# Optimization experiments

Measured on AMD Instinct MI355X. Metric: run time of the kernel, lower is better.

Reference implementation:

```python
import jax, jax.numpy as jnp
import numpy as np
from jax import lax

BN_EPS = 1e-5


def _gcn_layer(X, edge_index, W, sW, sb, gamma, beta):
    # X: (B, T, V, Fin). Self-loop linear + per-edge message + scatter-add.
    H = X @ sW + sb  # (B, T, V, Hd)
    src = edge_index[:, 0]
    dst = edge_index[:, 1]
    msgs = X[:, :, src, :] @ W  # (B, T, E, Hd) gather + GEMM
    H = H + jnp.zeros_like(H).at[:, :, dst, :].add(msgs)  # scatter-add over dst
    # BatchNorm1d applied per timestep in the torch loop -> stats over (B, V) per t
    mean = H.mean(axis=(0, 2), keepdims=True)
    var = H.var(axis=(0, 2), keepdims=True)  # biased var, as torch train-mode BN
    H = (H - mean) * lax.rsqrt(var + BN_EPS) * gamma + beta
    return jax.nn.relu(H)


def _conv_bn_relu(x, w, b, gamma, beta, dilation, padding):
    # x: (B, C, T), w: (O, I, K)
    y = lax.conv_general_dilated(x, w, window_strides=(1,),
                                 padding=[(padding, padding)],
                                 rhs_dilation=(dilation,),
                                 dimension_numbers=('NCH', 'OIH', 'NCH'))
    y = y + b[None, :, None]
    mean = y.mean(axis=(0, 2), keepdims=True)
    var = y.var(axis=(0, 2), keepdims=True)
    y = (y - mean) * lax.rsqrt(var + BN_EPS) * gamma[None, :, None] + beta[None, :, None]
    return jax.nn.relu(y)


def setup_inputs() -> dict:
    key = jax.random.key(0)
    ks = jax.random.split(key, 16)
    B, C, T, V, Hd, E, NC = 64, 3, 512, 25, 64, 48, 60
    s = 0.05
    inp = {
        'X': jax.random.normal(ks[0], (B, C, T, V), jnp.float32),
        'edge_index': jax.random.randint(ks[1], (E, 2), 0, V, jnp.int32),
        'W1': jax.random.normal(ks[2], (C, Hd), jnp.float32) * s,
        's1W': jax.random.normal(ks[3], (C, Hd), jnp.float32) * s,
        's1b': jax.random.normal(ks[4], (Hd,), jnp.float32) * s,
        'g1': jnp.ones((Hd,), jnp.float32),
        'b1': jnp.zeros((Hd,), jnp.float32),
        'W2': jax.random.normal(ks[5], (Hd, Hd), jnp.float32) * s,
        's2W': jax.random.normal(ks[6], (Hd, Hd), jnp.float32) * s,
        's2b': jax.random.normal(ks[7], (Hd,), jnp.float32) * s,
        'g2': jnp.ones((Hd,), jnp.float32),
        'b2': jnp.zeros((Hd,), jnp.float32),
        'c1W': jax.random.normal(ks[8], (64, V * Hd, 3), jnp.float32) * s,
        'c1b': jax.random.normal(ks[9], (64,), jnp.float32) * s,
        'tg1': jnp.ones((64,), jnp.float32),
        'tb1': jnp.zeros((64,), jnp.float32),
        'c2W': jax.random.normal(ks[10], (128, 64, 3), jnp.float32) * s,
        'c2b': jax.random.normal(ks[11], (128,), jnp.float32) * s,
        'tg2': jnp.ones((128,), jnp.float32),
        'tb2': jnp.zeros((128,), jnp.float32),
        'fcW': jax.random.normal(ks[12], (128, NC), jnp.float32) * s,
        'fcb': jax.random.normal(ks[13], (NC,), jnp.float32) * s,
    }
    return inp


def reference(X, edge_index, W1, s1W, s1b, g1, b1, W2, s2W, s2b, g2, b2,
              c1W, c1b, tg1, tb1, c2W, c2b, tg2, tb2, fcW, fcb):
    B, C, T, V = X.shape
    Xt = jnp.transpose(X, (0, 2, 3, 1))  # (B, T, V, C)
    H = _gcn_layer(Xt, edge_index, W1, s1W, s1b, g1, b1)  # (B, T, V, Hd)
    H = _gcn_layer(H, edge_index, W2, s2W, s2b, g2, b2)   # (B, T, V, Hd)
    Hd = H.shape[-1]
    # permute(0,2,3,1).reshape(B, V*Hd, T)
    z = jnp.transpose(H, (0, 2, 3, 1)).reshape(B, V * Hd, T)
    z = _conv_bn_relu(z, c1W, c1b, tg1, tb1, dilation=1, padding=1)
    z = _conv_bn_relu(z, c2W, c2b, tg2, tb2, dilation=2, padding=2)
    z = z.mean(axis=2)  # (B, 128)
    return z @ fcW + fcb
```

## Files before the change

### kernel.cpp

```cpp
#include <hip/hip_runtime.h>
#include <hip/hip_bf16.h>
#include <cstddef>

using bf16 = __hip_bfloat16;
typedef __attribute__((ext_vector_type(4)))  short bf16x4;
typedef __attribute__((ext_vector_type(8)))  short bf16x8;
typedef __attribute__((ext_vector_type(4)))  float f32x4;
typedef __attribute__((ext_vector_type(16))) float f32x16;
typedef __attribute__((ext_vector_type(2)))  unsigned int uint32x2;
typedef __attribute__((ext_vector_type(4)))  unsigned int uint32x4;

#define B_   64
#define T_   512
#define V_   25
#define HD_  64
#define E_   48
#define NC_  60

__device__ __forceinline__ bf16  f2b(float x){ return __float2bfloat16(x); }
__device__ __forceinline__ unsigned short f2bits(float x){ return __builtin_bit_cast(unsigned short, f2b(x)); }
__device__ __forceinline__ float bits2f(unsigned short s){ return __builtin_bit_cast(float, ((unsigned)s)<<16); }
__device__ __forceinline__ float rbf(float x){ return bits2f(f2bits(x)); }
__device__ __forceinline__ unsigned cvtpk(float lo, float hi){
  unsigned r;
  asm("v_cvt_pk_bf16_f32 %0, %1, %2" : "=v"(r) : "v"(lo), "v"(hi));
  return r;
}
__device__ __forceinline__ short cvt1(float x){ return (short)(unsigned short)cvtpk(x, x); }

__global__ void k_wt(const float* __restrict__ c1W, const float* __restrict__ c2W,
                     const float* __restrict__ s2W, const float* __restrict__ W2,
                     const float* __restrict__ s1W, const float* __restrict__ W1,
                     const int* __restrict__ ei,
                     bf16* __restrict__ Wb, bf16* __restrict__ Wb2,
                     bf16* __restrict__ WbB, bf16* __restrict__ W6f,
                     int* __restrict__ offs, int* __restrict__ lst)
{
  int i0 = blockIdx.x*blockDim.x + threadIdx.x, stride = gridDim.x*blockDim.x;
  if(blockIdx.x == 0 && threadIdx.x == 0){
    int cnt[V_], pos[V_];
    for(int v=0;v<V_;v++) cnt[v]=0;
    for(int e=0;e<E_;e++) cnt[ei[2*e+1]]++;
    int off = 0;
    for(int v=0;v<V_;v++){ offs[v]=off; pos[v]=off; off+=cnt[v]; }
    offs[V_] = off;
    for(int e=0;e<E_;e++){ int d = ei[2*e+1]; lst[pos[d]++] = ei[2*e+0]; }
  }
  for(int i = i0; i < 307200; i += stride){
    int hlo = i & 15, o = (i>>4)&63, kc = (i>>10)%12, v = i/12288;
    int ks = kc>>2, h = (kc&3)*16 + hlo;
    Wb[i] = f2b(c1W[(o*1600 + v*64 + h)*3 + ks]);
  }
  for(int i = i0; i < 24576; i += stride){
    int hlo = i & 15, o = (i>>4)&127, kc = i>>11;
    int ks = kc>>2, c = (kc&3)*16 + hlo;
    Wb2[i] = f2b(c2W[(o*64 + c)*3 + ks]);
  }
  for(int i = i0; i < 8192; i += stride){
    int j = i&7, l=(i>>3)&63, n=(i>>9)&3, kt=i>>11;
    int k = kt*32 + (l>>4)*8 + j;
    int h = n*16 + (l&15);
    float val = (k < 64) ? s2W[k*64 + h] : W2[(k-64)*64 + h];
    WbB[i] = f2b(val);
  }
  for(int i = i0; i < 2048; i += stride){
    int j = i&7, l=(i>>3)&63, n=(i>>9)&3;
    int k = (l>>4)*8 + j, h = n*16 + (l&15);
    float val = 0.f;
    if(k < 3) val = s1W[k*64 + h];
    else if(k < 6) val = W1[(k-3)*64 + h];
    W6f[i] = f2b(val);
  }
}

__global__ __launch_bounds__(512) void k_stats1(
    const float* __restrict__ X,
    const int* __restrict__ offs, const int* __restrict__ lst,
    float* __restrict__ gpart)
{
  int tid = threadIdx.x;
  int b = blockIdx.y, t0 = blockIdx.x*16;
  __shared__ short Xs[1248];
  __shared__ short Z6[3200];
  __shared__ unsigned char soc[32], slc[48];

  if(tid < V_+1) soc[tid] = (unsigned char)offs[tid];
  else if(tid >= 64 && tid < 64+E_) slc[tid-64] = (unsigned char)lst[tid-64];
  for(int i=tid; i<1248; i+=512){
    int c = i/416, r = i - c*416, tl = r/26, v = r - tl*26;
    short val = 0;
    if(v < 25) val = cvt1(X[((size_t)(b*3+c)*T_ + t0+tl)*V_ + v]);
    Xs[i] = val;
  }
  __syncthreads();
  if(tid < 400){
    int v = tid>>4, tl = tid&15, xb = tl*26;
    float a0=0.f, a1=0.f, a2=0.f;
    int e1 = soc[v+1];
    for(int e=soc[v]; e<e1; e++){
      int u = slc[e];
      a0 += bits2f((unsigned short)Xs[xb+u]);
      a1 += bits2f((unsigned short)Xs[416+xb+u]);
      a2 += bits2f((unsigned short)Xs[832+xb+u]);
    }
    unsigned p01 = cvtpk(a0, a1);
    bf16x8 z;
    z[0]=Xs[xb+v]; z[1]=Xs[416+xb+v]; z[2]=Xs[832+xb+v];
    z[3]=(short)p01; z[4]=(short)(p01>>16); z[5]=cvt1(a2);
    z[6]=0; z[7]=0;
    *(bf16x8*)&Z6[tid*8] = z;
  }
  __syncthreads();

  int t = tid>>5, item = tid&31;
  if(item < 27){
    int k = item, kk = -1;
    if(item >= 6){
      int r = item - 6; k = 0;
      while(r >= 6-k){ r -= 6-k; k++; }
      kk = k + r;
    }
    float acc = 0.f;
    for(int v=0;v<25;v++){
      const short* z = &Z6[(v*16 + t)*8];
      float a = bits2f((unsigned short)z[k]);
      if(kk < 0) acc += a;
      else acc += a * bits2f((unsigned short)z[kk]);
    }
    gpart[((size_t)blockIdx.x*64 + b)*432 + t*27 + item] = acc;
  }
}

__global__ __launch_bounds__(256) void k_bnfin1(
    const float* __restrict__ gpart,
    const float* __restrict__ s1W, const float* __restrict__ W1,
    const float* __restrict__ g, const float* __restrict__ bt,
    float* __restrict__ scale, float* __restrict__ shift)
{
  int tid = threadIdx.x;
  int t0 = blockIdx.x*4;
  int tx = t0 >> 4, tlb = t0 & 15;
  __shared__ float SM[4][27];
  __shared__ float Wsh[6][64];
  for(int i=tid; i<108; i+=256){
    int tl = i/27, item = i%27;
    float s = 0.f;
    for(int b=0;b<64;b++)
      s += gpart[((size_t)tx*64 + b)*432 + (tlb+tl)*27 + item];
    SM[tl][item] = s;
  }
  for(int i=tid; i<384; i+=256){
    int k = i>>6, h = i&63;
    float w = (k<3) ? s1W[k*64+h] : W1[(k-3)*64+h];
    Wsh[k][h] = rbf(w);
  }
  __syncthreads();
  int tl = tid>>6, h = tid&63;
  float w[6];
  #pragma unroll
  for(int k=0;k<6;k++) w[k] = Wsh[k][h];
  float lin = 0.f;
  #pragma unroll
  for(int k=0;k<6;k++) lin += w[k]*SM[tl][k];
  float qq = 0.f;
  int idx = 6;
  #pragma unroll
  for(int k=0;k<6;k++){
    #pragma unroll 6
    for(int kk=k;kk<6;kk++){
      float c = w[k]*w[kk];
      if(kk != k) c += c;
      qq += c*SM[tl][idx++];
    }
  }
  float m = lin * (1.0f/1600.0f);
  float v = qq * (1.0f/1600.0f) - m*m;
  float r = rsqrtf(fmaxf(v, 0.f) + 1e-5f);
  float sc = g[h]*r;
  scale[(t0+tl)*64 + h] = sc;
  shift[(t0+tl)*64 + h] = bt[h] - m*sc;
}

__global__ void k_bnfin_th(const float* __restrict__ part,
                           const float* __restrict__ g, const float* __restrict__ bt,
                           float* __restrict__ scale, float* __restrict__ shift)
{
  int i = blockIdx.x*blockDim.x + threadIdx.x;
  if(i < T_*HD_){
    int h = i & 63, t = i >> 6, bx = t >> 4, tl = t & 15;
    const float* p = part + ((size_t)bx*64)*2048 + tl*64 + h;
    float s = 0.f, q = 0.f;
    for(int b=0;b<64;b++){ s += p[(size_t)b*2048]; q += p[(size_t)b*2048 + 1024]; }
    float m = s * (1.0f/1600.0f);
    float v = q * (1.0f/1600.0f) - m*m;
    float r = rsqrtf(fmaxf(v, 0.f) + 1e-5f);
    float sc = g[h]*r;
    scale[i] = sc;
    shift[i] = bt[h] - m*sc;
  }
}

__global__ __launch_bounds__(512,4) void k_gcn2(
    const float* __restrict__ X,
    const float* __restrict__ scale1, const float* __restrict__ shift1,
    const bf16* __restrict__ W6f, const bf16* __restrict__ WbB,
    const int* __restrict__ offs, const int* __restrict__ lst,
    unsigned char* __restrict__ Hout, float* __restrict__ part)
{
  int tid = threadIdx.x, lane = tid & 63, wid = tid >> 6;
  int b = blockIdx.y, t0 = blockIdx.x*16;
  __shared__ short Zs[400*72];
  __shared__ short WbBs[8192];
  __shared__ unsigned int pss[1024];
  __shared__ unsigned char soc[32], slc[48];
  short* Z6 = Zs;
  short* Xs = Zs + 3200;

  bf16x8 w6[4];
  #pragma unroll
  for(int n=0;n<4;n++) w6[n] = *(const bf16x8*)&W6f[(n*64 + lane)*8];

  if(tid < V_+1) soc[tid] = (unsigned char)offs[tid];
  else if(tid >= 64 && tid < 64+E_) slc[tid-64] = (unsigned char)lst[tid-64];
  for(int i=tid; i<1024; i+=512){
    pss[i] = ((unsigned)f2bits(shift1[t0*64+i])<<16) | f2bits(scale1[t0*64+i]);
    *(bf16x8*)&WbBs[i*8] = *(const bf16x8*)&WbB[i*8];
  }
  for(int i=tid; i<1248; i+=512){
    int c = i/416, r = i - c*416, tl = r/26, v = r - tl*26;
    short val = 0;
    if(v < 25) val = cvt1(X[((size_t)(b*3+c)*T_ + t0+tl)*V_ + v]);
    Xs[i] = val;
  }
  __syncthreads();

  if(tid < 400){
    int v = tid>>4, tl = tid&15, xb = tl*26;
    float a0=0.f, a1=0.f, a2=0.f;
    int e1 = soc[v+1];
    for(int e=soc[v]; e<e1; e++){
      int u = slc[e];
      a0 += bits2f((unsigned short)Xs[xb+u]);
      a1 += bits2f((unsigned short)Xs[416+xb+u]);
      a2 += bits2f((unsigned short)Xs[832+xb+u]);
    }
    unsigned p01 = cvtpk(a0, a1);
    bf16x8 z;
    z[0]=Xs[xb+v]; z[1]=Xs[416+xb+v]; z[2]=Xs[832+xb+v];
    z[3]=(short)p01; z[4]=(short)(p01>>16); z[5]=cvt1(a2);
    z[6]=0; z[7]=0;
    *(bf16x8*)&Z6[tid*8] = z;
  }
  __syncthreads();

  f32x4 c1f[4][4] = {};
  #pragma unroll
  for(int vi=0; vi<4; vi++){
    int v = wid + vi*8;
    if(v < V_){
      bf16x8 af = {0,0,0,0,0,0,0,0};
      if(lane < 16) af = *(const bf16x8*)&Z6[(v*16 + lane)*8];
      #pragma unroll
      for(int n=0;n<4;n++)
        c1f[vi][n] = __builtin_amdgcn_mfma_f32_16x16x32_bf16(af, w6[n], c1f[vi][n], 0, 0, 0);
    }
  }
  __syncthreads();

  int l15 = lane & 15, tlb = (lane>>4)*4;
  #pragma unroll
  for(int vi=0; vi<4; vi++){
    int v = wid + vi*8;
    if(v < V_){
      #pragma unroll
      for(int n=0;n<4;n++){
        float y[4];
        #pragma unroll
        for(int j=0;j<4;j++){
          unsigned u = pss[(tlb+j)*64 + n*16 + l15];
          y[j] = fmaxf(c1f[vi][n][j]*bits2f((unsigned short)(u&0xffffu)) + bits2f((unsigned short)(u>>16)), 0.f);
        }
        unsigned p01 = cvtpk(y[0], y[1]), p23 = cvtpk(y[2], y[3]);
        short* base = &Zs[(v*16 + tlb)*72 + n*16 + l15];
        base[0]   = (short)p01;  base[72]  = (short)(p01>>16);
        base[144] = (short)p23;  base[216] = (short)(p23>>16);
      }
    }
  }
  __syncthreads();

  int cg = (lane>>4)*8;
  f32x4 accs[4][4] = {};
  #pragma unroll
  for(int vi=0; vi<4; vi++){
    int v = wid + vi*8;
    if(v < V_){
      const short* rowp = &Zs[(v*16 + l15)*72 + cg];
      bf16x8 a0 = *(const bf16x8*)rowp;
      bf16x8 a1 = *(const bf16x8*)(rowp + 32);
      float s0[8]={0,0,0,0,0,0,0,0}, s1[8]={0,0,0,0,0,0,0,0};
      int e1 = soc[v+1];
      for(int e=soc[v]; e<e1; e++){
        int u = slc[e];
        const short* np = &Zs[(u*16 + l15)*72 + cg];
        bf16x8 n0 = *(const bf16x8*)np;
        bf16x8 n1 = *(const bf16x8*)(np + 32);
        #pragma unroll
        for(int j=0;j<8;j++){ s0[j] += bits2f((unsigned short)n0[j]); s1[j] += bits2f((unsigned short)n1[j]); }
      }
      uint32x4 ua2, ua3;
      #pragma unroll
      for(int j=0;j<4;j++){ ua2[j] = cvtpk(s0[2*j], s0[2*j+1]); ua3[j] = cvtpk(s1[2*j], s1[2*j+1]); }
      bf16x8 a2 = __builtin_bit_cast(bf16x8, ua2);
      bf16x8 a3 = __builtin_bit_cast(bf16x8, ua3);
      #pragma unroll
      for(int n=0;n<4;n++){
        bf16x8 b0 = *(const bf16x8*)&WbBs[(( 0+n)*64 + lane)*8];
        accs[vi][n] = __builtin_amdgcn_mfma_f32_16x16x32_bf16(a0, b0, accs[vi][n], 0, 0, 0);
        bf16x8 b1 = *(const bf16x8*)&WbBs[(( 4+n)*64 + lane)*8];
        accs[vi][n] = __builtin_amdgcn_mfma_f32_16x16x32_bf16(a1, b1, accs[vi][n], 0, 0, 0);
        bf16x8 b2 = *(const bf16x8*)&WbBs[(( 8+n)*64 + lane)*8];
        accs[vi][n] = __builtin_amdgcn_mfma_f32_16x16x32_bf16(a2, b2, accs[vi][n], 0, 0, 0);
        bf16x8 b3 = *(const bf16x8*)&WbBs[((12+n)*64 + lane)*8];
        accs[vi][n] = __builtin_amdgcn_mfma_f32_16x16x32_bf16(a3, b3, accs[vi][n], 0, 0, 0);
      }
    }
  }
  __syncthreads();

  f32x4 ssum[4] = {}, ssq[4] = {};
  #pragma unroll
  for(int vi=0; vi<4; vi++){
    int v = wid + vi*8;
    if(v < V_){
      #pragma unroll
      for(int n=0;n<4;n++){
        float val[4];
        #pragma unroll
        for(int j=0;j<4;j++){
          val[j] = accs[vi][n][j];
          ssum[n][j] += val[j]; ssq[n][j] += val[j]*val[j];
        }
        unsigned p01 = cvtpk(val[0], val[1]), p23 = cvtpk(val[2], val[3]);
        short* base = &Zs[(tlb*25 + v)*72 + n*16 + l15];
        base[0]    = (short)p01;  base[1800] = (short)(p01>>16);
        base[3600] = (short)p23;  base[5400] = (short)(p23>>16);
      }
    }
  }
  __syncthreads();

  unsigned char* hbout = Hout + ((size_t)b*T_ + t0)*V_*64;
  for(int c=tid; c<3200; c+=512){
    bf16x8 o = *(const bf16x8*)&Zs[(c>>3)*72 + (c&7)*8];
    float f[8];
    #pragma unroll
    for(int j=0;j<8;j++) f[j] = bits2f((unsigned short)o[j]);
    int w0 = 0, w1 = 0;
    w0 = __builtin_amdgcn_cvt_pk_fp8_f32(f[0], f[1], w0, false);
    w0 = __builtin_amdgcn_cvt_pk_fp8_f32(f[2], f[3], w0, true);
    w1 = __builtin_amdgcn_cvt_pk_fp8_f32(f[4], f[5], w1, false);
    w1 = __builtin_amdgcn_cvt_pk_fp8_f32(f[6], f[7], w1, true);
    uint32x2 st; st.x = (unsigned)w0; st.y = (unsigned)w1;
    __builtin_nontemporal_store(st, (uint32x2*)&hbout[(size_t)c*8]);
  }
  __syncthreads();

  float* red = (float*)Zs;
  size_t pb = ((size_t)blockIdx.x*64 + blockIdx.y)*2048;
  #pragma unroll
  for(int n=0;n<4;n++)
    #pragma unroll
    for(int j=0;j<4;j++)
      red[wid*1024 + (tlb+j)*64 + n*16 + l15] = ssum[n][j];
  __syncthreads();
  for(int i=tid; i<1024; i+=512){
    float s = 0.f;
    #pragma unroll
    for(int w=0;w<8;w++) s += red[w*1024 + i];
    __builtin_nontemporal_store(s, &part[pb + i]);
  }
  __syncthreads();
  #pragma unroll
  for(int n=0;n<4;n++)
    #pragma unroll
    for(int j=0;j<4;j++)
      red[wid*1024 + (tlb+j)*64 + n*16 + l15] = ssq[n][j];
  __syncthreads();
  for(int i=tid; i<1024; i+=512){
    float q = 0.f;
    #pragma unroll
    for(int w=0;w<8;w++) q += red[w*1024 + i];
    __builtin_nontemporal_store(q, &part[pb + 1024 + i]);
  }
}

__device__ __forceinline__ uint32x2 loadH8(const unsigned char* H, int b, int v, int t0, int s){
  int ti = s>>3, h0 = (s&7)*8, t = t0-1+ti;
  uint32x2 r; r.x = 0u; r.y = 0u;
  if(t >= 0 && t < T_) r = *(const uint32x2*)&H[(((size_t)b*T_+t)*V_ + v)*HD_ + h0];
  return r;
}

__device__ __forceinline__ void xform_store(short* zbuf, const unsigned int* sshf, int s, uint32x2 raw){
  int ti = s>>3, h0 = (s&7)*8;
  uint4 u0 = *(const uint4*)&sshf[ti*64 + h0];
  uint4 u1 = *(const uint4*)&sshf[ti*64 + h0 + 4];
  unsigned int uu[8] = {u0.x,u0.y,u0.z,u0.w,u1.x,u1.y,u1.z,u1.w};
  float x[8];
  x[0] = __builtin_amdgcn_cvt_f32_fp8((int)raw.x, 0);
  x[1] = __builtin_amdgcn_cvt_f32_fp8((int)raw.x, 1);
  x[2] = __builtin_amdgcn_cvt_f32_fp8((int)raw.x, 2);
  x[3] = __builtin_amdgcn_cvt_f32_fp8((int)raw.x, 3);
  x[4] = __builtin_amdgcn_cvt_f32_fp8((int)raw.y, 0);
  x[5] = __builtin_amdgcn_cvt_f32_fp8((int)raw.y, 1);
  x[6] = __builtin_amdgcn_cvt_f32_fp8((int)raw.y, 2);
  x[7] = __builtin_amdgcn_cvt_f32_fp8((int)raw.y, 3);
  float r[8];
  #pragma unroll
  for(int j=0;j<8;j++){
    float scl = bits2f((unsigned short)(uu[j] & 0xffffu));
    float shf = bits2f((unsigned short)(uu[j] >> 16));
    r[j] = fmaxf(x[j]*scl + shf, 0.f);
  }
  uint32x4 u;
  #pragma unroll
  for(int j=0;j<4;j++) u[j] = cvtpk(r[2*j], r[2*j+1]);
  *(uint32x4*)&zbuf[ti*72 + h0] = u;
}

__global__ __launch_bounds__(256) void k_conv1(
    const unsigned char* __restrict__ H, const float* __restrict__ scale2, const float* __restrict__ shift2,
    const bf16* __restrict__ Wb, bf16* __restrict__ C1b, float* __restrict__ cpart1)
{
  int b = blockIdx.y, t0 = blockIdx.x*32, tid = threadIdx.x;
  int lane = tid & 63, w = tid >> 6;
  __shared__ unsigned int sshf[34*64];
  __shared__ short zs[2][2][34*72];

  for(int i = tid; i < 34*64; i += 256){
    int ti = i>>6, h = i&63, t = t0-1+ti;
    unsigned int u = 0;
    if(t >= 0 && t < T_){
      u = ((unsigned)f2bits(shift2[t*64+h])<<16) | f2bits(scale2[t*64+h]);
    }
    sshf[i] = u;
  }
  __syncthreads();

  {
    uint32x2 a0 = loadH8(H,b,0,t0,tid);
    uint32x2 b0 = loadH8(H,b,13,t0,tid);
    uint32x2 a1, b1; a1.x=a1.y=b1.x=b1.y=0u;
    if(tid<16){ a1 = loadH8(H,b,0,t0,tid+256); b1 = loadH8(H,b,13,t0,tid+256); }
    xform_store(&zs[0][0][0], sshf, tid, a0);
    xform_store(&zs[1][0][0], sshf, tid, b0);
    if(tid<16){ xform_store(&zs[0][0][0], sshf, tid+256, a1); xform_store(&zs[1][0][0], sshf, tid+256, b1); }
  }
  uint32x2 rA0 = loadH8(H,b,1,t0,tid), rB0 = loadH8(H,b,14,t0,tid);
  uint32x2 rA1, rB1; rA1.x=rA1.y=rB1.x=rB1.y=0u;
  if(tid<16){ rA1 = loadH8(H,b,1,t0,tid+256); rB1 = loadH8(H,b,14,t0,tid+256); }
  __syncthreads();

  int g = w >> 1;
  int o0 = (w & 1)*32;
  int vbase = g ? 13 : 0, nv = g ? 12 : 13;
  f32x16 acc = {};
  for(int i=0; i<13; i++){
    uint32x2 nA0, nA1, nB0, nB1;
    nA0.x=nA0.y=nA1.x=nA1.y=nB0.x=nB0.y=nB1.x=nB1.y=0u;
    if(i+2 < 13){
      nA0 = loadH8(H,b,i+2,t0,tid);
      if(tid<16) nA1 = loadH8(H,b,i+2,t0,tid+256);
    }
    if(i+2 < 12){
      nB0 = loadH8(H,b,13+i+2,t0,tid);
      if(tid<16) nB1 = loadH8(H,b,13+i+2,t0,tid+256);
    }
    if(i < nv){
      int v = vbase + i;
      const short* zbuf = &zs[g][i&1][0];
      #pragma unroll
      for(int kc=0; kc<12; kc++){
        int ks = kc>>2;
        bf16x8 af = *(const bf16x8*)&Wb[((v*12+kc)*64 + o0 + (lane&31))*16 + (lane>>5)*8];
        int row = (lane&31) + ks;
        int col = (kc&3)*16 + (lane>>5)*8;
        bf16x8 bfr = *(const bf16x8*)&zbuf[row*72 + col];
        acc = __builtin_amdgcn_mfma_f32_32x32x16_bf16(af, bfr, acc, 0, 0, 0);
      }
    }
    if(i+1 < 13){
      xform_store(&zs[0][(i+1)&1][0], sshf, tid, rA0);
      if(tid<16) xform_store(&zs[0][(i+1)&1][0], sshf, tid+256, rA1);
    }
    if(i+1 < 12){
      xform_store(&zs[1][(i+1)&1][0], sshf, tid, rB0);
      if(tid<16) xform_store(&zs[1][(i+1)&1][0], sshf, tid+256, rB1);
    }
    rA0=nA0; rA1=nA1; rB0=nB0; rB1=nB1;
    __syncthreads();
  }

  float* redB = (float*)&zs[0][0][0];
  short* Cs   = &zs[0][0][0] + 4224;
  if(g == 1){
    #pragma unroll
    for(int r=0;r<16;r++){
      int ol = (r&3) + 8*(r>>2) + 4*(lane>>5);
      redB[(w&1)*1056 + ol*33 + (lane&31)] = acc[r];
    }
  }
  __syncthreads();
  if(g == 0){
    #pragma unroll
    for(int r=0;r<16;r++){
      int ol = (r&3) + 8*(r>>2) + 4*(lane>>5);
      float val = acc[r] + redB[(w&1)*1056 + ol*33 + (lane&31)];
      Cs[((w&1)*32 + ol)*32 + (lane&31)] = cvt1(val);
    }
  }
  __syncthreads();

  {
    int o = tid>>2, tseg = (tid&3)*8;
    bf16x8 row = *(const bf16x8*)&Cs[o*32 + tseg];
    *(bf16x8*)&C1b[((size_t)b*64 + o)*T_ + t0 + tseg] = row;
  }
  if(tid < 64){
    float s = 0.f, q = 0.f;
    for(int t=0;t<32;t++){
      float v = bits2f((unsigned short)Cs[tid*32 + t]);
      s += v; q += v*v;
    }
    size_t pb = ((size_t)blockIdx.y*16 + blockIdx.x)*128;
    cpart1[pb + tid] = s;
    cpart1[pb + 64 + tid] = q;
  }
}

__global__ __launch_bounds__(256) void k_redch(const float* __restrict__ cpart,
    const float* __restrict__ g, const float* __restrict__ bt,
    float* __restrict__ scale, float* __restrict__ shift, int nch, int nblk, float inv_count)
{
  int o = blockIdx.x, tid = threadIdx.x;
  float s = 0.f, q = 0.f;
  for(int blk=tid; blk<nblk; blk+=256){
    s += cpart[(size_t)blk*2*nch + o];
    q += cpart[(size_t)blk*2*nch + nch + o];
  }
  for(int off=32; off; off>>=1){ s += __shfl_down(s, off); q += __shfl_down(q, off); }
  __shared__ float rs[4], rq[4];
  if((tid&63)==0){ rs[tid>>6]=s; rq[tid>>6]=q; }
  __syncthreads();
  if(tid==0){
    s = rs[0]+rs[1]+rs[2]+rs[3]; q = rq[0]+rq[1]+rq[2]+rq[3];
    float m = s*inv_count;
    float v = q*inv_count - m*m;
    float r = rsqrtf(fmaxf(v, 0.f) + 1e-5f);
    float sc = g[o]*r;
    scale[o] = sc; shift[o] = bt[o] - m*sc;
  }
}

__global__ __launch_bounds__(256) void k_conv2(
    const bf16* __restrict__ C1b, const float* __restrict__ scale3, const float* __restrict__ shift3,
    const bf16* __restrict__ Wb2, short* __restrict__ C2b, float* __restrict__ cpart)
{
  int b = blockIdx.y, t0 = blockIdx.x*64, tid = threadIdx.x;
  int lane = tid & 63, w = tid >> 6;
  __shared__ short zT[68*72];
  __shared__ float scl[64], shf[64];
  __shared__ float rpart[4][16][2][2];
  if(tid < 64){ scl[tid]=scale3[tid]; shf[tid]=shift3[tid]; }
  __syncthreads();
  for(int i=tid; i<4352; i+=256){
    int c = i/68, r = i%68, t = t0 - 2 + r;
    float val = 0.f;
    if(t >= 0 && t < T_) val = fmaxf(bits2f((unsigned short)__builtin_bit_cast(short, C1b[((size_t)b*64+c)*T_ + t]))*scl[c] + shf[c], 0.f);
    zT[r*72 + c] = cvt1(val);
  }
  __syncthreads();
  int o0 = w*32;
  float sr[16], qr[16];
  #pragma unroll
  for(int r=0;r<16;r++){ sr[r]=0.f; qr[r]=0.f; }
  #pragma unroll
  for(int tt=0; tt<2; tt++){
    int twv = tt*32;
    f32x16 acc = {};
    #pragma unroll
    for(int kc=0; kc<12; kc++){
      bf16x8 af = *(const bf16x8*)&Wb2[((kc*128) + o0 + (lane&31))*16 + (lane>>5)*8];
      bf16x8 bfr = *(const bf16x8*)&zT[(twv + (lane&31) + 2*(kc>>2))*72 + (kc&3)*16 + (lane>>5)*8];
      acc = __builtin_amdgcn_mfma_f32_32x32x16_bf16(af, bfr, acc, 0, 0, 0);
    }
    int t = t0 + twv + (lane&31);
    #pragma unroll
    for(int r=0;r<16;r++){
      int o = o0 + (r&3) + 8*(r>>2) + 4*(lane>>5);
      float y = acc[r];
      C2b[((size_t)b*128 + o)*T_ + t] = cvt1(y);
      sr[r] += y; qr[r] += y*y;
    }
  }
  #pragma unroll
  for(int r=0;r<16;r++){
    float s = sr[r], q = qr[r];
    #pragma unroll
    for(int m=1;m<=16;m<<=1){ s += __shfl_xor(s, m); q += __shfl_xor(q, m); }
    if((lane&31)==0){ rpart[w][r][lane>>5][0]=s; rpart[w][r][lane>>5][1]=q; }
  }
  __syncthreads();
  if(tid < 128){
    int wv = tid>>5, r = (tid>>1)&15, hf = tid&1;
    int o = wv*32 + (r&3) + 8*(r>>2) + 4*hf;
    size_t pb = ((size_t)(blockIdx.y*8 + blockIdx.x))*256;
    cpart[pb + o]       = rpart[wv][r][hf][0];
    cpart[pb + 128 + o] = rpart[wv][r][hf][1];
  }
}

__global__ __launch_bounds__(256) void k_head(
    const short* __restrict__ C2b, const float* __restrict__ scale4, const float* __restrict__ shift4,
    const float* __restrict__ fcW, const float* __restrict__ fcb, float* __restrict__ out)
{
  int b = blockIdx.x, tid = threadIdx.x;
  __shared__ float mean[128];
  __shared__ float ms[256];
  int ch = tid >> 1, p = tid & 1;
  float scl = scale4[ch], shf = shift4[ch];
  const short* src = C2b + ((size_t)b*128 + ch)*T_ + p*256;
  float s = 0.f;
  for(int i=0;i<32;i++){
    bf16x8 v8 = *(const bf16x8*)&src[i*8];
    #pragma unroll
    for(int j=0;j<8;j++) s += fmaxf(bits2f((unsigned short)v8[j])*scl + shf, 0.f);
  }
  ms[tid] = s;
  __syncthreads();
  if(tid < 128) mean[tid] = (ms[2*tid] + ms[2*tid+1]) * (1.0f/512.0f);
  __syncthreads();
  if(tid < NC_){
    float acc = fcb[tid];
    for(int c=0;c<128;c++) acc += mean[c]*fcW[c*NC_ + tid];
    out[b*NC_ + tid] = acc;
  }
}

extern "C" void kernel_launch(void* const* d_in, const int* in_sizes, int n_in,
                              void* d_out, int out_size, void* d_ws, size_t ws_size,
                              hipStream_t stream)
{
  const float* X   = (const float*)d_in[0];
  const int*   ei  = (const int*)  d_in[1];
  const float* W1  = (const float*)d_in[2];
  const float* s1W = (const float*)d_in[3];
  const float* g1  = (const float*)d_in[5];
  const float* b1  = (const float*)d_in[6];
  const float* W2  = (const float*)d_in[7];
  const float* s2W = (const float*)d_in[8];
  const float* g2  = (const float*)d_in[10];
  const float* b2  = (const float*)d_in[11];
  const float* c1W = (const float*)d_in[12];
  const float* tg1 = (const float*)d_in[14];
  const float* tb1 = (const float*)d_in[15];
  const float* c2W = (const float*)d_in[16];
  const float* tg2 = (const float*)d_in[18];
  const float* tb2 = (const float*)d_in[19];
  const float* fcW = (const float*)d_in[20];
  const float* fcb = (const float*)d_in[21];

  char* ws = (char*)d_ws;
  unsigned char* H = (unsigned char*)(ws);
  bf16*  C1b    = (bf16*) (ws + 104857600);
  float* cpart1 = (float*)(ws + 109051904);
  float* cpart2 = (float*)(ws + 109576192);
  float* part   = (float*)(ws + 113246208);
  float* gpart  = part;
  short* C2b    = (short*)part;
  bf16*  Wb     = (bf16*) (ws + 130023424);
  bf16*  Wb2    = (bf16*) (ws + 131252224);
  bf16*  WbB    = (bf16*) (ws + 131350528);
  float* stats  = (float*)(ws + 131366912);
  bf16*  W6f    = (bf16*) (stats);
  float* scale1 = stats + 131456; float* shift1 = scale1 + 32768;
  float* scale2 = shift1 + 32768; float* shift2 = scale2 + 32768;
  float* scale3 = shift2 + 32768; float* shift3 = scale3 + 64;
  float* scale4 = shift3 + 64;    float* shift4 = scale4 + 128;
  int* csr_off = (int*)(shift4 + 128);
  int* csr_lst = csr_off + 32;

  k_wt<<<256, 256, 0, stream>>>(c1W, c2W, s2W, W2, s1W, W1, ei, Wb, Wb2, WbB, W6f, csr_off, csr_lst);

  k_stats1<<<dim3(T_/16, B_), 512, 0, stream>>>(X, csr_off, csr_lst, gpart);
  k_bnfin1<<<128, 256, 0, stream>>>(gpart, s1W, W1, g1, b1, scale1, shift1);
  k_gcn2<<<dim3(T_/16, B_), 512, 0, stream>>>(X, scale1, shift1, W6f, WbB, csr_off, csr_lst, H, part);
  k_bnfin_th<<<128, 256, 0, stream>>>(part, g2, b2, scale2, shift2);
  k_conv1<<<dim3(16, B_), 256, 0, stream>>>(H, scale2, shift2, Wb, C1b, cpart1);
  k_redch<<<64, 256, 0, stream>>>(cpart1, tg1, tb1, scale3, shift3, 64, 1024, 1.0f/32768.0f);
  k_conv2<<<dim3(8, B_), 256, 0, stream>>>(C1b, scale3, shift3, Wb2, C2b, cpart2);
  k_redch<<<128, 256, 0, stream>>>(cpart2, tg2, tb2, scale4, shift4, 128, 512, 1.0f/32768.0f);
  k_head<<<B_, 256, 0, stream>>>(C2b, scale4, shift4, fcW, fcb, (float*)d_out);
}
```

Before: 201.9 us.

## Use LDS atomics for GCN stat reduction and split head kernel over time

Result: slower. 361.6 us (+79.1%).

```diff
diff --git a/kernel.cpp b/kernel.cpp
--- a/kernel.cpp
+++ b/kernel.cpp
@@ -367,32 +367,19 @@
   __syncthreads();
 
   float* red = (float*)Zs;
-  size_t pb = ((size_t)blockIdx.x*64 + blockIdx.y)*2048;
+  for(int i=tid; i<2048; i+=512) red[i] = 0.f;
+  __syncthreads();
   #pragma unroll
   for(int n=0;n<4;n++)
     #pragma unroll
-    for(int j=0;j<4;j++)
-      red[wid*1024 + (tlb+j)*64 + n*16 + l15] = ssum[n][j];
-  __syncthreads();
-  for(int i=tid; i<1024; i+=512){
-    float s = 0.f;
-    #pragma unroll
-    for(int w=0;w<8;w++) s += red[w*1024 + i];
-    __builtin_nontemporal_store(s, &part[pb + i]);
-  }
-  __syncthreads();
-  #pragma unroll
-  for(int n=0;n<4;n++)
-    #pragma unroll
-    for(int j=0;j<4;j++)
-      red[wid*1024 + (tlb+j)*64 + n*16 + l15] = ssq[n][j];
-  __syncthreads();
-  for(int i=tid; i<1024; i+=512){
-    float q = 0.f;
-    #pragma unroll
-    for(int w=0;w<8;w++) q += red[w*1024 + i];
-    __builtin_nontemporal_store(q, &part[pb + 1024 + i]);
-  }
+    for(int j=0;j<4;j++){
+      atomicAdd(&red[(tlb+j)*64 + n*16 + l15], ssum[n][j]);
+      atomicAdd(&red[1024 + (tlb+j)*64 + n*16 + l15], ssq[n][j]);
+    }
+  __syncthreads();
+  size_t pb = ((size_t)blockIdx.x*64 + blockIdx.y)*2048;
+  for(int i=tid; i<2048; i+=512)
+    __builtin_nontemporal_store(red[i], &part[pb + i]);
 }
 
 __device__ __forceinline__ uint32x2 loadH8(const unsigned char* H, int b, int v, int t0, int s){
@@ -621,25 +608,34 @@
   }
 }
 
-__global__ __launch_bounds__(256) void k_head(
+__global__ __launch_bounds__(256) void k_head1(
     const short* __restrict__ C2b, const float* __restrict__ scale4, const float* __restrict__ shift4,
-    const float* __restrict__ fcW, const float* __restrict__ fcb, float* __restrict__ out)
-{
-  int b = blockIdx.x, tid = threadIdx.x;
-  __shared__ float mean[128];
+    float* __restrict__ hpart)
+{
+  int b = blockIdx.y, q = blockIdx.x, tid = threadIdx.x;
   __shared__ float ms[256];
   int ch = tid >> 1, p = tid & 1;
   float scl = scale4[ch], shf = shift4[ch];
-  const short* src = C2b + ((size_t)b*128 + ch)*T_ + p*256;
+  const short* src = C2b + ((size_t)b*128 + ch)*T_ + q*128 + p*64;
   float s = 0.f;
-  for(int i=0;i<32;i++){
+  for(int i=0;i<8;i++){
     bf16x8 v8 = *(const bf16x8*)&src[i*8];
     #pragma unroll
     for(int j=0;j<8;j++) s += fmaxf(bits2f((unsigned short)v8[j])*scl + shf, 0.f);
   }
   ms[tid] = s;
   __syncthreads();
-  if(tid < 128) mean[tid] = (ms[2*tid] + ms[2*tid+1]) * (1.0f/512.0f);
+  if(tid < 128) hpart[((size_t)b*4 + q)*128 + tid] = ms[2*tid] + ms[2*tid+1];
+}
+
+__global__ __launch_bounds__(128) void k_head2(
+    const float* __restrict__ hpart, const float* __restrict__ fcW, const float* __restrict__ fcb,
+    float* __restrict__ out)
+{
+  int b = blockIdx.x, tid = threadIdx.x;
+  __shared__ float mean[128];
+  const float* hp = hpart + (size_t)b*512;
+  mean[tid] = (hp[tid] + hp[128+tid] + hp[256+tid] + hp[384+tid]) * (1.0f/512.0f);
   __syncthreads();
   if(tid < NC_){
     float acc = fcb[tid];
@@ -679,6 +675,7 @@
   float* part   = (float*)(ws + 113246208);
   float* gpart  = part;
   short* C2b    = (short*)part;
+  float* hpart  = cpart1;
   bf16*  Wb     = (bf16*) (ws + 130023424);
   bf16*  Wb2    = (bf16*) (ws + 131252224);
   bf16*  WbB    = (bf16*) (ws + 131350528);
@@ -701,5 +698,6 @@
   k_redch<<<64, 256, 0, stream>>>(cpart1, tg1, tb1, scale3, shift3, 64, 1024, 1.0f/32768.0f);
   k_conv2<<<dim3(8, B_), 256, 0, stream>>>(C1b, scale3, shift3, Wb2, C2b, cpart2);
   k_redch<<<128, 256, 0, stream>>>(cpart2, tg2, tb2, scale4, shift4, 128, 512, 1.0f/32768.0f);
-  k_head<<<B_, 256, 0, stream>>>(C2b, scale4, shift4, fcW, fcb, (float*)d_out);
-}
+  k_head1<<<dim3(4, B_), 256, 0, stream>>>(C2b, scale4, shift4, hpart);
+  k_head2<<<B_, 128, 0, stream>>>(hpart, fcW, fcb, (float*)d_out);
+}
```
